# Optimization experiments

Hardware: AMD Instinct MI355X
Metric: run time of the kernel (lower is better)

## Reference

```python
import jax, jax.numpy as jnp
import numpy as np

D = 4096   # feature_dim
L = 24     # num_vision_layers
H = 8      # num_heads
HD = D // H
R = D // 4 # reduced_dim


def _ln(x, g, b, eps=1e-5):
    m = jnp.mean(x, -1, keepdims=True)
    v = jnp.var(x, -1, keepdims=True)
    return (x - m) * jax.lax.rsqrt(v + eps) * g + b


def setup_inputs() -> dict:
    key = jax.random.key(0)
    ks = jax.random.split(key, 16)
    B, T, N = 1, 128, 576
    def W(k, shape, s=0.02):
        return jax.random.normal(k, shape, jnp.float32) * s
    inp = {
        'text': jax.random.normal(ks[0], (B, T, D), jnp.float32),
        'feats': jax.random.normal(ks[1], (L, B, N, D), jnp.float32),
        'W1_w': W(ks[2], (R, 3 * D)), 'W1_b': jnp.zeros((R,), jnp.float32),
        'Wc_w': W(ks[3], (D, R)), 'Wc_b': jnp.zeros((D,), jnp.float32),
        'Wi_w': W(ks[4], (D, R)), 'Wi_b': jnp.zeros((D,), jnp.float32),
        'Wf_w': W(ks[5], (D, R)), 'Wf_b': jnp.zeros((D,), jnp.float32),
        'bc': jnp.zeros((D,), jnp.float32),
        'bi': jnp.zeros((D,), jnp.float32),
        'bf': jnp.zeros((D,), jnp.float32),
        'g1_w': W(ks[6], (D, D)), 'g1_b': jnp.zeros((D,), jnp.float32),
        'g2_w': W(ks[7], (D, D)), 'g2_b': jnp.zeros((D,), jnp.float32),
        'Wq_w': W(ks[8], (D, D)), 'Wq_b': jnp.zeros((D,), jnp.float32),
        'Wk_w': W(ks[9], (D, D)), 'Wk_b': jnp.zeros((D,), jnp.float32),
        'Wo_w': W(ks[10], (D, D)), 'Wo_b': jnp.zeros((D,), jnp.float32),
        'qn_g': jnp.ones((D,), jnp.float32), 'qn_b': jnp.zeros((D,), jnp.float32),
        'kn_g': jnp.ones((D,), jnp.float32), 'kn_b': jnp.zeros((D,), jnp.float32),
        'on_g': jnp.ones((D,), jnp.float32), 'on_b': jnp.zeros((D,), jnp.float32),
    }
    return inp


def reference(text, feats, W1_w, W1_b, Wc_w, Wc_b, Wi_w, Wi_b, Wf_w, Wf_b,
              bc, bi, bf, g1_w, g1_b, g2_w, g2_b, Wq_w, Wq_b, Wk_w, Wk_b,
              Wo_w, Wo_b, qn_g, qn_b, kn_g, kn_b, on_g, on_b):
    B, T, _ = text.shape
    N = feats.shape[2]
    text_global = jnp.mean(text, axis=1)      # [B, D]
    y = jnp.mean(feats, axis=2)               # [L, B, D]

    # DSU recurrence over L layers (shared weights) via scan
    def step(c_prev, y_l):
        cpn = jax.nn.sigmoid(jax.lax.stop_gradient(c_prev))
        comb = jnp.concatenate([cpn, y_l, text_global], axis=-1)  # [B, 3D]
        s = jax.nn.relu(comb @ W1_w.T + W1_b)                     # [B, R]
        c_tilde = jnp.tanh(s @ Wc_w.T + Wc_b + bc)
        ig = jax.nn.sigmoid(s @ Wi_w.T + Wi_b + bi)
        fg = jax.nn.sigmoid(s @ Wf_w.T + Wf_b + bf)
        c = fg * c_prev + ig * c_tilde
        return c, c

    _, ctx = jax.lax.scan(step, jnp.zeros_like(text_global), y)   # [L, B, D]

    # Spatial gate, vectorized over all L layers (context is detached)
    c_sg = jax.lax.stop_gradient(ctx)[:, :, None, :]              # [L, B, 1, D]
    h = jax.nn.gelu((c_sg + feats) @ g1_w.T + g1_b, approximate=False)
    gate = jax.nn.sigmoid(h @ g2_w.T + g2_b)
    refreshed = feats * gate                                      # [L, B, N, D]

    # Q / K / V
    Q = _ln(text @ Wq_w.T + Wq_b, qn_g, qn_b)
    Q = Q.reshape(B, T, H, HD).transpose(0, 2, 1, 3)              # [B, H, T, HD]
    K = _ln(refreshed @ Wk_w.T + Wk_b, kn_g, kn_b)                # [L, B, N, D]
    K_all = K.reshape(L, B, N, H, HD).transpose(1, 3, 0, 2, 4).reshape(B, H, L * N, HD)
    V_all = refreshed.reshape(L, B, N, H, HD).transpose(1, 3, 0, 2, 4).reshape(B, H, L * N, HD)

    scale = (HD ** 0.5) * (L ** 0.5)
    scores = jnp.einsum('bhtd,bhsd->bhts', Q, K_all) / scale
    attn = jax.nn.softmax(scores, axis=-1)
    att = jnp.einsum('bhts,bhsd->bhtd', attn, V_all)
    att = att.transpose(0, 2, 1, 3).reshape(B, T, D)
    out = _ln(att @ Wo_w.T + Wo_b, on_g, on_b)
    return out
```

## Files before the change

kernel.cpp:

```cpp
#include <hip/hip_runtime.h>

#define USH unsigned short

__device__ __forceinline__ float bf2f(USH u) {
    return __uint_as_float(((unsigned int)u) << 16);
}
__device__ __forceinline__ float bfbits2f(unsigned int b) {
    return __uint_as_float(b << 16);
}
__device__ __forceinline__ USH f2bf(float f) {
    unsigned int x = __float_as_uint(f);
    x += 0x7fffu + ((x >> 16) & 1u);
    return (USH)(x >> 16);
}
__device__ __forceinline__ unsigned int pack2bf(float a, float b) {
    return (unsigned int)f2bf(a) | ((unsigned int)f2bf(b) << 16);
}
__device__ __forceinline__ float sigmoidf_(float x) { return 1.0f / (1.0f + expf(-x)); }

typedef __bf16 bf16x8 __attribute__((ext_vector_type(8)));
typedef float floatx4 __attribute__((ext_vector_type(4)));

#define GLOAD_LDS16(g, l) __builtin_amdgcn_global_load_lds( \
    (const __attribute__((address_space(1))) void*)(g),     \
    (__attribute__((address_space(3))) void*)(l), 16, 0, 0)

enum { EPI_SCORES = 0, EPI_GELU = 1, EPI_GATE = 2, EPI_PLAIN = 3 };

template <int EPI, bool WF32>
__global__ __launch_bounds__(256)
void gemm_bt(const USH* __restrict__ A, int lda, long long sAz,
             const void* __restrict__ Wv, int ldw, long long sWz,
             void* __restrict__ Cout, int ldc, long long sCz,
             const float* __restrict__ bias, const float* __restrict__ fmul,
             float alpha, int Kd)
{
    __shared__ USH As[128 * 32];
    __shared__ USH Ws[128 * 32];
    const int z = blockIdx.z;
    A += (size_t)z * (size_t)sAz;
    const USH* Wb = (const USH*)Wv + (size_t)z * (size_t)sWz;
    const float* Wf = (const float*)Wv;
    const int m0 = blockIdx.y * 128;
    const int n0 = blockIdx.x * 128;
    const int tid = threadIdx.x;
    const int lane = tid & 63;
    const int wid = tid >> 6;
    const int wm = (wid >> 1) * 64;
    const int wn = (wid & 1) * 64;
    const int q = lane >> 4;
    const int r = lane & 15;

    floatx4 acc[4][4] = {};

    const int c0 = wid * 2;
    const int grow = c0 * 16 + (lane >> 2);
    const int gcol = (lane & 3) * 8;
    const USH* apA0 = A + (size_t)(m0 + grow) * lda + gcol;
    const USH* apA1 = apA0 + (size_t)16 * lda;
    USH* lA0 = &As[c0 * 512];
    USH* lA1 = &As[(c0 + 1) * 512];
    const USH* apW0 = Wb + (size_t)(n0 + grow) * ldw + gcol;
    const USH* apW1 = apW0 + (size_t)16 * ldw;
    USH* lW0 = &Ws[c0 * 512];
    USH* lW1 = &Ws[(c0 + 1) * 512];

    const int frow = tid >> 1;
    const int fcol = (tid & 1) * 16;
    const float* wpf = Wf + (size_t)(n0 + frow) * ldw + fcol;
    USH* wsw = &Ws[frow * 32 + fcol];

    for (int k0 = 0; k0 < Kd; k0 += 32) {
        GLOAD_LDS16(apA0 + k0, lA0);
        GLOAD_LDS16(apA1 + k0, lA1);
        if (WF32) {
            float4 f0 = *reinterpret_cast<const float4*>(wpf + k0);
            float4 f1 = *reinterpret_cast<const float4*>(wpf + k0 + 4);
            float4 f2 = *reinterpret_cast<const float4*>(wpf + k0 + 8);
            float4 f3 = *reinterpret_cast<const float4*>(wpf + k0 + 12);
            uint4 w0, w1;
            w0.x = pack2bf(f0.x, f0.y); w0.y = pack2bf(f0.z, f0.w);
            w0.z = pack2bf(f1.x, f1.y); w0.w = pack2bf(f1.z, f1.w);
            w1.x = pack2bf(f2.x, f2.y); w1.y = pack2bf(f2.z, f2.w);
            w1.z = pack2bf(f3.x, f3.y); w1.w = pack2bf(f3.z, f3.w);
            *reinterpret_cast<uint4*>(wsw) = w0;
            *reinterpret_cast<uint4*>(wsw + 8) = w1;
        } else {
            GLOAD_LDS16(apW0 + k0, lW0);
            GLOAD_LDS16(apW1 + k0, lW1);
        }
        __syncthreads();
        bf16x8 af[4], wf4[4];
#pragma unroll
        for (int i = 0; i < 4; i++)
            af[i] = *reinterpret_cast<const bf16x8*>(&As[(wm + i * 16 + r) * 32 + q * 8]);
#pragma unroll
        for (int j = 0; j < 4; j++)
            wf4[j] = *reinterpret_cast<const bf16x8*>(&Ws[(wn + j * 16 + r) * 32 + q * 8]);
#pragma unroll
        for (int i = 0; i < 4; i++)
#pragma unroll
            for (int j = 0; j < 4; j++)
                acc[i][j] = __builtin_amdgcn_mfma_f32_16x16x32_bf16(af[i], wf4[j], acc[i][j], 0, 0, 0);
        __syncthreads();
    }

#pragma unroll
    for (int j = 0; j < 4; j++) {
        const int col = n0 + wn + j * 16 + r;
        const float bv = (EPI == EPI_SCORES) ? 0.f : bias[col];
#pragma unroll
        for (int i = 0; i < 4; i++) {
            const int row0 = m0 + wm + i * 16 + q * 4;
#pragma unroll
            for (int rr = 0; rr < 4; rr++) {
                const int row = row0 + rr;
                float v = acc[i][j][rr];
                if (EPI == EPI_SCORES) {
                    ((float*)Cout)[(size_t)z * (size_t)sCz + (size_t)row * ldc + col] = v * alpha;
                } else if (EPI == EPI_GELU) {
                    v += bv;
                    float g = 0.5f * v * (1.0f + erff(v * 0.7071067811865475f));
                    ((USH*)Cout)[(size_t)row * ldc + col] = f2bf(g);
                } else if (EPI == EPI_GATE) {
                    v += bv;
                    float gate = 1.0f / (1.0f + expf(-v));
                    float o = gate * fmul[(size_t)row * ldc + col];
                    ((USH*)Cout)[(size_t)row * ldc + col] = f2bf(o);
                } else {
                    ((USH*)Cout)[(size_t)row * ldc + col] = f2bf(v + bv);
                }
            }
        }
    }
}

__global__ __launch_bounds__(256)
void means_k(const float* __restrict__ text, const float* __restrict__ feats,
             float* __restrict__ tg, float* __restrict__ yv, float* __restrict__ cst,
             float* __restrict__ scs)
{
    const int d = blockIdx.x * 256 + threadIdx.x;
    const int z = blockIdx.y;
    if (z < 24) {
        const float* f = feats + (size_t)z * 576 * 4096 + d;
        float s = 0.f;
        for (int n = 0; n < 576; n++) s += f[(size_t)n * 4096];
        yv[z * 4096 + d] = s * (1.0f / 576.0f);
    } else if (z == 24) {
        float s = 0.f;
        for (int t = 0; t < 128; t++) s += text[(size_t)t * 4096 + d];
        tg[d] = s * (1.0f / 128.0f);
    } else {
        cst[d] = 0.f;
        scs[d] = 0.5f;
    }
}

__global__ __launch_bounds__(256)
void f32_to_bf16(const float* __restrict__ src, USH* __restrict__ dst)
{
    const size_t base = ((size_t)blockIdx.x * 256 + threadIdx.x) * 8;
    float4 f0 = *reinterpret_cast<const float4*>(src + base);
    float4 f1 = *reinterpret_cast<const float4*>(src + base + 4);
    uint4 ov;
    ov.x = pack2bf(f0.x, f0.y); ov.y = pack2bf(f0.z, f0.w);
    ov.z = pack2bf(f1.x, f1.y); ov.w = pack2bf(f1.z, f1.w);
    *reinterpret_cast<uint4*>(dst + base) = ov;
}

__global__ __launch_bounds__(256)
void dsu_pre(const float* __restrict__ W1w, const float* __restrict__ W1b,
             const float* __restrict__ yv, const float* __restrict__ tg,
             float* __restrict__ pre)
{
    const int rrow = blockIdx.x;
    const float* w = W1w + (size_t)rrow * 12288;
    const int tid = threadIdx.x;
    float wy[16];
    float at = 0.f;
#pragma unroll
    for (int i = 0; i < 16; i++) {
        const int k = tid + i * 256;
        wy[i] = w[4096 + k];
        at += w[8192 + k] * tg[k];
    }
#pragma unroll
    for (int o = 32; o > 0; o >>= 1) at += __shfl_down(at, o, 64);
    __shared__ float red[4];
    __shared__ float tgs;
    if ((tid & 63) == 0) red[tid >> 6] = at;
    __syncthreads();
    if (tid == 0) tgs = red[0] + red[1] + red[2] + red[3] + W1b[rrow];
    for (int l = 0; l < 24; l++) {
        const float* y = yv + (size_t)l * 4096;
        float a = 0.f;
#pragma unroll
        for (int i = 0; i < 16; i++) a += wy[i] * y[tid + i * 256];
#pragma unroll
        for (int o = 32; o > 0; o >>= 1) a += __shfl_down(a, o, 64);
        __syncthreads();
        if ((tid & 63) == 0) red[tid >> 6] = a;
        __syncthreads();
        if (tid == 0) pre[l * 1024 + rrow] = red[0] + red[1] + red[2] + red[3] + tgs;
    }
}

__global__ __launch_bounds__(256)
void dsu_s1(const float* __restrict__ W1w, const float* __restrict__ scs,
            const float* __restrict__ pre_l, float* __restrict__ sv)
{
    const int rrow = blockIdx.x;
    const float* w = W1w + (size_t)rrow * 12288;
    const int tid = threadIdx.x;
    float acc = 0.f;
#pragma unroll
    for (int i = 0; i < 16; i++) {
        const int k = tid + i * 256;
        acc += w[k] * scs[k];
    }
#pragma unroll
    for (int o = 32; o > 0; o >>= 1) acc += __shfl_down(acc, o, 64);
    __shared__ float red[4];
    if ((tid & 63) == 0) red[tid >> 6] = acc;
    __syncthreads();
    if (tid == 0) {
        float t = red[0] + red[1] + red[2] + red[3] + pre_l[rrow];
        sv[rrow] = fmaxf(t, 0.f);
    }
}

__global__ __launch_bounds__(256)
void dsu_s2(const float* __restrict__ Wc, const float* __restrict__ Wcb,
            const float* __restrict__ Wi, const float* __restrict__ Wib,
            const float* __restrict__ Wf, const float* __restrict__ Wfb,
            const float* __restrict__ bc, const float* __restrict__ bi,
            const float* __restrict__ bfv,
            const float* __restrict__ sv, float* __restrict__ c,
            float* __restrict__ ctx_l, float* __restrict__ scs)
{
    const int d = blockIdx.x;
    const int tid = threadIdx.x;
    float a0 = 0.f, a1 = 0.f, a2 = 0.f;
    for (int k = tid; k < 1024; k += 256) {
        float s = sv[k];
        a0 += Wc[(size_t)d * 1024 + k] * s;
        a1 += Wi[(size_t)d * 1024 + k] * s;
        a2 += Wf[(size_t)d * 1024 + k] * s;
    }
#pragma unroll
    for (int o = 32; o > 0; o >>= 1) {
        a0 += __shfl_down(a0, o, 64);
        a1 += __shfl_down(a1, o, 64);
        a2 += __shfl_down(a2, o, 64);
    }
    __shared__ float red[3][4];
    if ((tid & 63) == 0) {
        red[0][tid >> 6] = a0; red[1][tid >> 6] = a1; red[2][tid >> 6] = a2;
    }
    __syncthreads();
    if (tid == 0) {
        float A0 = red[0][0] + red[0][1] + red[0][2] + red[0][3];
        float A1 = red[1][0] + red[1][1] + red[1][2] + red[1][3];
        float A2 = red[2][0] + red[2][1] + red[2][2] + red[2][3];
        float ct = tanhf(A0 + Wcb[d] + bc[d]);
        float ig = sigmoidf_(A1 + Wib[d] + bi[d]);
        float fg = sigmoidf_(A2 + Wfb[d] + bfv[d]);
        float cn = fg * c[d] + ig * ct;
        c[d] = cn;
        ctx_l[d] = cn;
        scs[d] = sigmoidf_(cn);
    }
}

__global__ __launch_bounds__(256)
void make_x(const float* __restrict__ feats, const float* __restrict__ ctx,
            USH* __restrict__ X)
{
    const size_t base = ((size_t)blockIdx.x * 256 + threadIdx.x) * 8;
    const int row = (int)(base >> 12);
    const int l = row / 576;
    const float* cr = ctx + (size_t)l * 4096 + (base & 4095);
    float4 f0 = *reinterpret_cast<const float4*>(feats + base);
    float4 f1 = *reinterpret_cast<const float4*>(feats + base + 4);
    uint4 ov;
    ov.x = pack2bf(f0.x + cr[0], f0.y + cr[1]);
    ov.y = pack2bf(f0.z + cr[2], f0.w + cr[3]);
    ov.z = pack2bf(f1.x + cr[4], f1.y + cr[5]);
    ov.w = pack2bf(f1.z + cr[6], f1.w + cr[7]);
    *reinterpret_cast<uint4*>(X + base) = ov;
}

template <bool OUTF32>
__global__ __launch_bounds__(256)
void ln_rows(const USH* __restrict__ in, void* __restrict__ out,
             const float* __restrict__ g, const float* __restrict__ b)
{
    const int row = blockIdx.x;
    const USH* x = in + (size_t)row * 4096;
    const int tid = threadIdx.x;
    float vals[16];
    float s = 0.f, ss = 0.f;
#pragma unroll
    for (int i = 0; i < 16; i++) {
        float v = bf2f(x[tid + i * 256]);
        vals[i] = v; s += v; ss += v * v;
    }
#pragma unroll
    for (int off = 32; off > 0; off >>= 1) {
        s += __shfl_down(s, off, 64);
        ss += __shfl_down(ss, off, 64);
    }
    __shared__ float rs[4], rss[4];
    __shared__ float stats[2];
    if ((tid & 63) == 0) { rs[tid >> 6] = s; rss[tid >> 6] = ss; }
    __syncthreads();
    if (tid == 0) {
        float S = rs[0] + rs[1] + rs[2] + rs[3];
        float SS = rss[0] + rss[1] + rss[2] + rss[3];
        float mean = S * (1.0f / 4096.0f);
        float var = SS * (1.0f / 4096.0f) - mean * mean;
        stats[0] = mean;
        stats[1] = rsqrtf(var + 1e-5f);
    }
    __syncthreads();
    const float mean = stats[0], rstd = stats[1];
#pragma unroll
    for (int i = 0; i < 16; i++) {
        const int cidx = tid + i * 256;
        float v = (vals[i] - mean) * rstd * g[cidx] + b[cidx];
        if (OUTF32) ((float*)out)[(size_t)row * 4096 + cidx] = v;
        else ((USH*)out)[(size_t)row * 4096 + cidx] = f2bf(v);
    }
}

__global__ __launch_bounds__(256)
void softmax_rows(const float* __restrict__ scores, USH* __restrict__ probs)
{
    const int row = blockIdx.x;
    const float* x = scores + (size_t)row * 13824;
    USH* p = probs + (size_t)row * 13824;
    const int tid = threadIdx.x;
    float mx = -1e30f;
    for (int i = tid; i < 13824; i += 256) mx = fmaxf(mx, x[i]);
#pragma unroll
    for (int off = 32; off > 0; off >>= 1) mx = fmaxf(mx, __shfl_down(mx, off, 64));
    __shared__ float rm[4];
    __shared__ float bm, bs;
    if ((tid & 63) == 0) rm[tid >> 6] = mx;
    __syncthreads();
    if (tid == 0) bm = fmaxf(fmaxf(rm[0], rm[1]), fmaxf(rm[2], rm[3]));
    __syncthreads();
    const float M = bm;
    float sum = 0.f;
    for (int i = tid; i < 13824; i += 256) sum += expf(x[i] - M);
#pragma unroll
    for (int off = 32; off > 0; off >>= 1) sum += __shfl_down(sum, off, 64);
    if ((tid & 63) == 0) rm[tid >> 6] = sum;
    __syncthreads();
    if (tid == 0) bs = 1.0f / (rm[0] + rm[1] + rm[2] + rm[3]);
    __syncthreads();
    const float inv = bs;
    for (int i = tid; i < 13824; i += 256) p[i] = f2bf(expf(x[i] - M) * inv);
}

__global__ __launch_bounds__(256)
void pv_kernel(const USH* __restrict__ P, const USH* __restrict__ V,
               USH* __restrict__ att)
{
    const int h = blockIdx.z;
    const int d0 = blockIdx.x * 64;
    const int t0 = blockIdx.y * 32;
    const int tid = threadIdx.x;
    const int tl = tid >> 3;
    const int dg = tid & 7;
    __shared__ USH Ps[32][72];
    __shared__ USH Vs[64][72];
    float acc[8] = {0.f, 0.f, 0.f, 0.f, 0.f, 0.f, 0.f, 0.f};

    for (int sc = 0; sc < 13824; sc += 64) {
        {
            const USH* pp = P + (size_t)(h * 128 + t0 + (tid >> 3)) * 13824 + sc + (tid & 7) * 8;
            uint4 v = *reinterpret_cast<const uint4*>(pp);
            *reinterpret_cast<uint4*>(&Ps[tid >> 3][(tid & 7) * 8]) = v;
        }
        {
            const USH* vp = V + (size_t)(sc + (tid >> 2)) * 4096 + h * 512 + d0 + (tid & 3) * 16;
            uint4 v0 = *reinterpret_cast<const uint4*>(vp);
            uint4 v1 = *reinterpret_cast<const uint4*>(vp + 8);
            *reinterpret_cast<uint4*>(&Vs[tid >> 2][(tid & 3) * 16]) = v0;
            *reinterpret_cast<uint4*>(&Vs[tid >> 2][(tid & 3) * 16 + 8]) = v1;
        }
        __syncthreads();
#pragma unroll 8
        for (int s8 = 0; s8 < 64; s8++) {
            float pv = bf2f(Ps[tl][s8]);
            uint4 raw = *reinterpret_cast<const uint4*>(&Vs[s8][dg * 8]);
            acc[0] += pv * bfbits2f(raw.x & 0xffffu);
            acc[1] += pv * bfbits2f(raw.x >> 16);
            acc[2] += pv * bfbits2f(raw.y & 0xffffu);
            acc[3] += pv * bfbits2f(raw.y >> 16);
            acc[4] += pv * bfbits2f(raw.z & 0xffffu);
            acc[5] += pv * bfbits2f(raw.z >> 16);
            acc[6] += pv * bfbits2f(raw.w & 0xffffu);
            acc[7] += pv * bfbits2f(raw.w >> 16);
        }
        __syncthreads();
    }
    USH* o = att + (size_t)(t0 + tl) * 4096 + h * 512 + d0 + dg * 8;
    uint4 ov;
    ov.x = pack2bf(acc[0], acc[1]);
    ov.y = pack2bf(acc[2], acc[3]);
    ov.z = pack2bf(acc[4], acc[5]);
    ov.w = pack2bf(acc[6], acc[7]);
    *reinterpret_cast<uint4*>(o) = ov;
}

extern "C" void kernel_launch(void* const* d_in, const int* in_sizes, int n_in,
                              void* d_out, int out_size, void* d_ws, size_t ws_size,
                              hipStream_t stream)
{
    const float* text = (const float*)d_in[0];
    const float* feats = (const float*)d_in[1];
    const float* W1w = (const float*)d_in[2];
    const float* W1b = (const float*)d_in[3];
    const float* Wcw = (const float*)d_in[4];
    const float* Wcb = (const float*)d_in[5];
    const float* Wiw = (const float*)d_in[6];
    const float* Wib = (const float*)d_in[7];
    const float* Wfw = (const float*)d_in[8];
    const float* Wfb = (const float*)d_in[9];
    const float* bc  = (const float*)d_in[10];
    const float* bi  = (const float*)d_in[11];
    const float* bfv = (const float*)d_in[12];
    const float* g1w = (const float*)d_in[13];
    const float* g1b = (const float*)d_in[14];
    const float* g2w = (const float*)d_in[15];
    const float* g2b = (const float*)d_in[16];
    const float* Wqw = (const float*)d_in[17];
    const float* Wqb = (const float*)d_in[18];
    const float* Wkw = (const float*)d_in[19];
    const float* Wkb = (const float*)d_in[20];
    const float* Wow = (const float*)d_in[21];
    const float* Wob = (const float*)d_in[22];
    const float* qng = (const float*)d_in[23];
    const float* qnb = (const float*)d_in[24];
    const float* kng = (const float*)d_in[25];
    const float* knb = (const float*)d_in[26];
    const float* ong = (const float*)d_in[27];
    const float* onb = (const float*)d_in[28];

    char* base = (char*)d_ws;
    size_t off = 0;
    auto take = [&](size_t nbytes) -> char* {
        char* p = base + off;
        off += (nbytes + 255) & ~(size_t)255;
        return p;
    };
    const size_t BIG = (size_t)13824 * 4096 * 2;
    USH* P1 = (USH*)take(BIG);
    USH* P2 = (USH*)take(BIG);
    USH* P3 = (USH*)take(BIG);
    float* tg  = (float*)take(4096 * 4);
    float* yv  = (float*)take(24 * 4096 * 4);
    float* cst = (float*)take(4096 * 4);
    float* scs = (float*)take(4096 * 4);
    float* sv  = (float*)take(1024 * 4);
    float* pre = (float*)take(24 * 1024 * 4);
    float* ctx = (float*)take(24 * 4096 * 4);
    USH* textb = (USH*)take((size_t)128 * 4096 * 2);
    USH* Qb   = (USH*)take((size_t)128 * 4096 * 2);
    USH* attb = (USH*)take((size_t)128 * 4096 * 2);
    USH* opre = (USH*)take((size_t)128 * 4096 * 2);
    USH* wb   = (USH*)take((size_t)4096 * 4096 * 2);
    float* scores = (float*)P2;
    USH* probs = (USH*)((char*)P2 + (size_t)8 * 128 * 13824 * 4);
    (void)ws_size; (void)in_sizes; (void)n_in; (void)out_size;

    means_k<<<dim3(16, 26), 256, 0, stream>>>(text, feats, tg, yv, cst, scs);
    f32_to_bf16<<<256, 256, 0, stream>>>(text, textb);
    dsu_pre<<<1024, 256, 0, stream>>>(W1w, W1b, yv, tg, pre);

    for (int l = 0; l < 24; l++) {
        dsu_s1<<<1024, 256, 0, stream>>>(W1w, scs, pre + (size_t)l * 1024, sv);
        dsu_s2<<<4096, 256, 0, stream>>>(Wcw, Wcb, Wiw, Wib, Wfw, Wfb, bc, bi, bfv,
                                         sv, cst, ctx + (size_t)l * 4096, scs);
    }

    make_x<<<27648, 256, 0, stream>>>(feats, ctx, P1);
    f32_to_bf16<<<8192, 256, 0, stream>>>(g1w, wb);
    gemm_bt<EPI_GELU, false><<<dim3(32, 108, 1), 256, 0, stream>>>(
        P1, 4096, 0, wb, 4096, 0, P2, 4096, 0, g1b, nullptr, 1.f, 4096);
    f32_to_bf16<<<8192, 256, 0, stream>>>(g2w, wb);
    gemm_bt<EPI_GATE, false><<<dim3(32, 108, 1), 256, 0, stream>>>(
        P2, 4096, 0, wb, 4096, 0, P3, 4096, 0, g2b, feats, 1.f, 4096);

    f32_to_bf16<<<8192, 256, 0, stream>>>(Wkw, wb);
    gemm_bt<EPI_PLAIN, false><<<dim3(32, 108, 1), 256, 0, stream>>>(
        P3, 4096, 0, wb, 4096, 0, P1, 4096, 0, Wkb, nullptr, 1.f, 4096);
    ln_rows<false><<<13824, 256, 0, stream>>>(P1, P1, kng, knb);

    gemm_bt<EPI_PLAIN, true><<<dim3(32, 1, 1), 256, 0, stream>>>(
        textb, 4096, 0, Wqw, 4096, 0, Qb, 4096, 0, Wqb, nullptr, 1.f, 4096);
    ln_rows<false><<<128, 256, 0, stream>>>(Qb, Qb, qng, qnb);

    const float alpha = 0.00902109753f;
    gemm_bt<EPI_SCORES, false><<<dim3(108, 1, 8), 256, 0, stream>>>(
        Qb, 4096, 512, P1, 4096, 512, scores, 13824, (long long)128 * 13824,
        nullptr, nullptr, alpha, 512);

    softmax_rows<<<1024, 256, 0, stream>>>(scores, probs);
    pv_kernel<<<dim3(8, 4, 8), 256, 0, stream>>>(probs, P3, attb);

    gemm_bt<EPI_PLAIN, true><<<dim3(32, 1, 1), 256, 0, stream>>>(
        attb, 4096, 0, Wow, 4096, 0, opre, 4096, 0, Wob, nullptr, 1.f, 4096);
    ln_rows<true><<<128, 256, 0, stream>>>(opre, (float*)d_out, ong, onb);
}
```

Baseline: 4.310 ms.

## Run PV through split-K MFMA GEMM and double-buffer GEMM LDS tiles

Replaces the scalar FMA pv_kernel with a transpose of V into a [D, S] layout, a split-K batched MFMA GEMM over 8 heads × 8 chunks of 1728 keys writing fp32 partials, and a small reduction kernel that sums the partials and converts to bf16. The shared GEMM kernel also gets double-buffered LDS with global-to-LDS loads for the next k-slice issued before computing the current one, plus a two-level z index for the split-K batching. The PV change is meant to remove a slow CUDA-core loop over 13824 keys. It costs an extra transpose pass over V and an fp32 partial buffer. The double buffering is meant to overlap memory latency with MFMA work in all the large GEMMs, at the cost of twice the LDS per block.

```diff
diff --git a/kernel.cpp b/kernel.cpp
--- a/kernel.cpp
+++ b/kernel.cpp
@@ -29,17 +29,19 @@
 
 template <int EPI, bool WF32>
 __global__ __launch_bounds__(256)
-void gemm_bt(const USH* __restrict__ A, int lda, long long sAz,
-             const void* __restrict__ Wv, int ldw, long long sWz,
+void gemm_bt(const USH* __restrict__ A, int lda, long long sAz, long long sAz2, int zdiv,
+             const void* __restrict__ Wv, int ldw, long long sWz, long long sWz2,
              void* __restrict__ Cout, int ldc, long long sCz,
              const float* __restrict__ bias, const float* __restrict__ fmul,
              float alpha, int Kd)
 {
-    __shared__ USH As[128 * 32];
-    __shared__ USH Ws[128 * 32];
+    __shared__ USH As[2][128 * 32];
+    __shared__ USH Ws[2][128 * 32];
     const int z = blockIdx.z;
-    A += (size_t)z * (size_t)sAz;
-    const USH* Wb = (const USH*)Wv + (size_t)z * (size_t)sWz;
+    const int z1 = z / zdiv;
+    const int z2 = z % zdiv;
+    A += (size_t)z1 * (size_t)sAz + (size_t)z2 * (size_t)sAz2;
+    const USH* Wb = (const USH*)Wv + (size_t)z1 * (size_t)sWz + (size_t)z2 * (size_t)sWz2;
     const float* Wf = (const float*)Wv;
     const int m0 = blockIdx.y * 128;
     const int n0 = blockIdx.x * 128;
@@ -58,22 +60,22 @@
     const int gcol = (lane & 3) * 8;
     const USH* apA0 = A + (size_t)(m0 + grow) * lda + gcol;
     const USH* apA1 = apA0 + (size_t)16 * lda;
-    USH* lA0 = &As[c0 * 512];
-    USH* lA1 = &As[(c0 + 1) * 512];
+    USH* lA0 = &As[0][c0 * 512];
+    USH* lA1 = &As[0][(c0 + 1) * 512];
     const USH* apW0 = Wb + (size_t)(n0 + grow) * ldw + gcol;
     const USH* apW1 = apW0 + (size_t)16 * ldw;
-    USH* lW0 = &Ws[c0 * 512];
-    USH* lW1 = &Ws[(c0 + 1) * 512];
+    USH* lW0 = &Ws[0][c0 * 512];
+    USH* lW1 = &Ws[0][(c0 + 1) * 512];
 
     const int frow = tid >> 1;
     const int fcol = (tid & 1) * 16;
     const float* wpf = Wf + (size_t)(n0 + frow) * ldw + fcol;
-    USH* wsw = &Ws[frow * 32 + fcol];
-
-    for (int k0 = 0; k0 < Kd; k0 += 32) {
-        GLOAD_LDS16(apA0 + k0, lA0);
-        GLOAD_LDS16(apA1 + k0, lA1);
-        if (WF32) {
+    USH* wsw = &Ws[0][frow * 32 + fcol];
+
+    auto stage = [&](int k0, int b) {
+        GLOAD_LDS16(apA0 + k0, lA0 + b * 4096);
+        GLOAD_LDS16(apA1 + k0, lA1 + b * 4096);
+        if constexpr (WF32) {
             float4 f0 = *reinterpret_cast<const float4*>(wpf + k0);
             float4 f1 = *reinterpret_cast<const float4*>(wpf + k0 + 4);
             float4 f2 = *reinterpret_cast<const float4*>(wpf + k0 + 8);
@@ -83,26 +85,44 @@
             w0.z = pack2bf(f1.x, f1.y); w0.w = pack2bf(f1.z, f1.w);
             w1.x = pack2bf(f2.x, f2.y); w1.y = pack2bf(f2.z, f2.w);
             w1.z = pack2bf(f3.x, f3.y); w1.w = pack2bf(f3.z, f3.w);
-            *reinterpret_cast<uint4*>(wsw) = w0;
-            *reinterpret_cast<uint4*>(wsw + 8) = w1;
+            *reinterpret_cast<uint4*>(wsw + b * 4096) = w0;
+            *reinterpret_cast<uint4*>(wsw + b * 4096 + 8) = w1;
         } else {
-            GLOAD_LDS16(apW0 + k0, lW0);
-            GLOAD_LDS16(apW1 + k0, lW1);
+            GLOAD_LDS16(apW0 + k0, lW0 + b * 4096);
+            GLOAD_LDS16(apW1 + k0, lW1 + b * 4096);
         }
-        __syncthreads();
+    };
+
+    auto compute = [&](const USH* Asb, const USH* Wsb) {
         bf16x8 af[4], wf4[4];
 #pragma unroll
         for (int i = 0; i < 4; i++)
-            af[i] = *reinterpret_cast<const bf16x8*>(&As[(wm + i * 16 + r) * 32 + q * 8]);
+            af[i] = *reinterpret_cast<const bf16x8*>(&Asb[(wm + i * 16 + r) * 32 + q * 8]);
 #pragma unroll
         for (int j = 0; j < 4; j++)
-            wf4[j] = *reinterpret_cast<const bf16x8*>(&Ws[(wn + j * 16 + r) * 32 + q * 8]);
+            wf4[j] = *reinterpret_cast<const bf16x8*>(&Wsb[(wn + j * 16 + r) * 32 + q * 8]);
 #pragma unroll
         for (int i = 0; i < 4; i++)
 #pragma unroll
             for (int j = 0; j < 4; j++)
                 acc[i][j] = __builtin_amdgcn_mfma_f32_16x16x32_bf16(af[i], wf4[j], acc[i][j], 0, 0, 0);
-        __syncthreads();
+    };
+
+    stage(0, 0);
+    asm volatile("s_waitcnt vmcnt(0) lgkmcnt(0)" ::: "memory");
+    __builtin_amdgcn_s_barrier();
+
+    for (int k0 = 0; k0 < Kd; k0 += 64) {
+        stage(k0 + 32, 1);
+        compute(&As[0][0], &Ws[0][0]);
+        asm volatile("s_waitcnt vmcnt(0) lgkmcnt(0)" ::: "memory");
+        __builtin_amdgcn_s_barrier();
+        if (k0 + 64 < Kd) stage(k0 + 64, 0);
+        compute(&As[1][0], &Ws[1][0]);
+        if (k0 + 64 < Kd) {
+            asm volatile("s_waitcnt vmcnt(0) lgkmcnt(0)" ::: "memory");
+            __builtin_amdgcn_s_barrier();
+        }
     }
 
 #pragma unroll
@@ -170,6 +190,55 @@
 }
 
 __global__ __launch_bounds__(256)
+void transpose_bf16(const USH* __restrict__ src, USH* __restrict__ dst)
+{
+    __shared__ USH T[64][72];
+    const int s0 = blockIdx.x * 64;
+    const int d0 = blockIdx.y * 64;
+    const int tid = threadIdx.x;
+    const int rr = tid >> 3;
+    const int c8 = (tid & 7) * 8;
+#pragma unroll
+    for (int i = 0; i < 2; i++) {
+        const int row = rr + i * 32;
+        uint4 v = *reinterpret_cast<const uint4*>(src + (size_t)(s0 + row) * 4096 + d0 + c8);
+        *reinterpret_cast<uint4*>(&T[row][c8]) = v;
+    }
+    __syncthreads();
+#pragma unroll
+    for (int i = 0; i < 2; i++) {
+        const int drow = rr + i * 32;
+        USH tmp[8];
+#pragma unroll
+        for (int j = 0; j < 8; j++) tmp[j] = T[c8 + j][drow];
+        *reinterpret_cast<uint4*>(dst + (size_t)(d0 + drow) * 13824 + s0 + c8) =
+            *reinterpret_cast<const uint4*>(tmp);
+    }
+}
+
+__global__ __launch_bounds__(256)
+void pv_reduce(const float* __restrict__ part, USH* __restrict__ att)
+{
+    const int idx = blockIdx.x * 256 + threadIdx.x;
+    const size_t o = (size_t)idx * 4;
+    const int t = (int)(o >> 12);
+    const int col = (int)(o & 4095);
+    const int h = col >> 9;
+    const int d = col & 511;
+    const float* p = part + (size_t)h * 8 * 65536 + t * 512 + d;
+    float4 s = {0.f, 0.f, 0.f, 0.f};
+#pragma unroll
+    for (int kc = 0; kc < 8; kc++) {
+        float4 v = *reinterpret_cast<const float4*>(p + (size_t)kc * 65536);
+        s.x += v.x; s.y += v.y; s.z += v.z; s.w += v.w;
+    }
+    uint2 ov;
+    ov.x = pack2bf(s.x, s.y);
+    ov.y = pack2bf(s.z, s.w);
+    *reinterpret_cast<uint2*>(att + o) = ov;
+}
+
+__global__ __launch_bounds__(256)
 void dsu_pre(const float* __restrict__ W1w, const float* __restrict__ W1b,
              const float* __restrict__ yv, const float* __restrict__ tg,
              float* __restrict__ pre)
@@ -236,8 +305,8 @@
             const float* __restrict__ Wf, const float* __restrict__ Wfb,
             const float* __restrict__ bc, const float* __restrict__ bi,
             const float* __restrict__ bfv,
-            const float* __restrict__ sv, float* __restrict__ c,
-            float* __restrict__ ctx_l, float* __restrict__ scs)
+             const float* __restrict__ sv, float* __restrict__ c,
+             float* __restrict__ ctx_l, float* __restrict__ scs)
 {
     const int d = blockIdx.x;
     const int tid = threadIdx.x;
@@ -362,58 +431,6 @@
     __syncthreads();
     const float inv = bs;
     for (int i = tid; i < 13824; i += 256) p[i] = f2bf(expf(x[i] - M) * inv);
-}
-
-__global__ __launch_bounds__(256)
-void pv_kernel(const USH* __restrict__ P, const USH* __restrict__ V,
-               USH* __restrict__ att)
-{
-    const int h = blockIdx.z;
-    const int d0 = blockIdx.x * 64;
-    const int t0 = blockIdx.y * 32;
-    const int tid = threadIdx.x;
-    const int tl = tid >> 3;
-    const int dg = tid & 7;
-    __shared__ USH Ps[32][72];
-    __shared__ USH Vs[64][72];
-    float acc[8] = {0.f, 0.f, 0.f, 0.f, 0.f, 0.f, 0.f, 0.f};
-
-    for (int sc = 0; sc < 13824; sc += 64) {
-        {
-            const USH* pp = P + (size_t)(h * 128 + t0 + (tid >> 3)) * 13824 + sc + (tid & 7) * 8;
-            uint4 v = *reinterpret_cast<const uint4*>(pp);
-            *reinterpret_cast<uint4*>(&Ps[tid >> 3][(tid & 7) * 8]) = v;
-        }
-        {
-            const USH* vp = V + (size_t)(sc + (tid >> 2)) * 4096 + h * 512 + d0 + (tid & 3) * 16;
-            uint4 v0 = *reinterpret_cast<const uint4*>(vp);
-            uint4 v1 = *reinterpret_cast<const uint4*>(vp + 8);
-            *reinterpret_cast<uint4*>(&Vs[tid >> 2][(tid & 3) * 16]) = v0;
-            *reinterpret_cast<uint4*>(&Vs[tid >> 2][(tid & 3) * 16 + 8]) = v1;
-        }
-        __syncthreads();
-#pragma unroll 8
-        for (int s8 = 0; s8 < 64; s8++) {
-            float pv = bf2f(Ps[tl][s8]);
-            uint4 raw = *reinterpret_cast<const uint4*>(&Vs[s8][dg * 8]);
-            acc[0] += pv * bfbits2f(raw.x & 0xffffu);
-            acc[1] += pv * bfbits2f(raw.x >> 16);
-            acc[2] += pv * bfbits2f(raw.y & 0xffffu);
-            acc[3] += pv * bfbits2f(raw.y >> 16);
-            acc[4] += pv * bfbits2f(raw.z & 0xffffu);
-            acc[5] += pv * bfbits2f(raw.z >> 16);
-            acc[6] += pv * bfbits2f(raw.w & 0xffffu);
-            acc[7] += pv * bfbits2f(raw.w >> 16);
-        }
-        __syncthreads();
-    }
-    USH* o = att + (size_t)(t0 + tl) * 4096 + h * 512 + d0 + dg * 8;
-    uint4 ov;
-    ov.x = pack2bf(acc[0], acc[1]);
-    ov.y = pack2bf(acc[2], acc[3]);
-    ov.z = pack2bf(acc[4], acc[5]);
-    ov.w = pack2bf(acc[6], acc[7]);
-    *reinterpret_cast<uint4*>(o) = ov;
 }
 
 extern "C" void kernel_launch(void* const* d_in, const int* in_sizes, int n_in,
@@ -475,6 +492,8 @@
     USH* wb   = (USH*)take((size_t)4096 * 4096 * 2);
     float* scores = (float*)P2;
     USH* probs = (USH*)((char*)P2 + (size_t)8 * 128 * 13824 * 4);
+    USH* vT = P1;
+    float* pvpart = (float*)wb;
     (void)ws_size; (void)in_sizes; (void)n_in; (void)out_size;
 
     means_k<<<dim3(16, 26), 256, 0, stream>>>(text, feats, tg, yv, cst, scs);
@@ -490,29 +509,35 @@
     make_x<<<27648, 256, 0, stream>>>(feats, ctx, P1);
     f32_to_bf16<<<8192, 256, 0, stream>>>(g1w, wb);
     gemm_bt<EPI_GELU, false><<<dim3(32, 108, 1), 256, 0, stream>>>(
-        P1, 4096, 0, wb, 4096, 0, P2, 4096, 0, g1b, nullptr, 1.f, 4096);
+        P1, 4096, 0, 0, 1, wb, 4096, 0, 0, P2, 4096, 0, g1b, nullptr, 1.f, 4096);
     f32_to_bf16<<<8192, 256, 0, stream>>>(g2w, wb);
     gemm_bt<EPI_GATE, false><<<dim3(32, 108, 1), 256, 0, stream>>>(
-        P2, 4096, 0, wb, 4096, 0, P3, 4096, 0, g2b, feats, 1.f, 4096);
+        P2, 4096, 0, 0, 1, wb, 4096, 0, 0, P3, 4096, 0, g2b, feats, 1.f, 4096);
 
     f32_to_bf16<<<8192, 256, 0, stream>>>(Wkw, wb);
     gemm_bt<EPI_PLAIN, false><<<dim3(32, 108, 1), 256, 0, stream>>>(
-        P3, 4096, 0, wb, 4096, 0, P1, 4096, 0, Wkb, nullptr, 1.f, 4096);
+        P3, 4096, 0, 0, 1, wb, 4096, 0, 0, P1, 4096, 0, Wkb, nullptr, 1.f, 4096);
     ln_rows<false><<<13824, 256, 0, stream>>>(P1, P1, kng, knb);
 
     gemm_bt<EPI_PLAIN, true><<<dim3(32, 1, 1), 256, 0, stream>>>(
-        textb, 4096, 0, Wqw, 4096, 0, Qb, 4096, 0, Wqb, nullptr, 1.f, 4096);
+        textb, 4096, 0, 0, 1, Wqw, 4096, 0, 0, Qb, 4096, 0, Wqb, nullptr, 1.f, 4096);
     ln_rows<false><<<128, 256, 0, stream>>>(Qb, Qb, qng, qnb);
 
     const float alpha = 0.00902109753f;
     gemm_bt<EPI_SCORES, false><<<dim3(108, 1, 8), 256, 0, stream>>>(
-        Qb, 4096, 512, P1, 4096, 512, scores, 13824, (long long)128 * 13824,
+        Qb, 4096, 512, 0, 1, P1, 4096, 512, 0, scores, 13824, (long long)128 * 13824,
         nullptr, nullptr, alpha, 512);
 
+    transpose_bf16<<<dim3(216, 64), 256, 0, stream>>>(P3, vT);
     softmax_rows<<<1024, 256, 0, stream>>>(scores, probs);
-    pv_kernel<<<dim3(8, 4, 8), 256, 0, stream>>>(probs, P3, attb);
+    gemm_bt<EPI_SCORES, false><<<dim3(4, 1, 64), 256, 0, stream>>>(
+        probs, 13824, (long long)128 * 13824, 1728, 8,
+        vT, 13824, (long long)512 * 13824, 1728,
+        pvpart, 512, 65536,
+        nullptr, nullptr, 1.0f, 1728);
+    pv_reduce<<<512, 256, 0, stream>>>(pvpart, attb);
 
     gemm_bt<EPI_PLAIN, true><<<dim3(32, 1, 1), 256, 0, stream>>>(
-        attb, 4096, 0, Wow, 4096, 0, opre, 4096, 0, Wob, nullptr, 1.f, 4096);
+        attb, 4096, 0, 0, 1, Wow, 4096, 0, 0, opre, 4096, 0, Wob, nullptr, 1.f, 4096);
     ln_rows<true><<<128, 256, 0, stream>>>(opre, (float*)d_out, ong, onb);
 }
```

After: 3.950 ms. 8.4% less time.
